# Kernel optimization log

Measured on AMD Instinct MI355X. Metric: run time of the kernel, lower is better.

## Reference

```python
import jax, jax.numpy as jnp
import numpy as np

CAPACITY_GAMMA = 0.5

def setup_inputs() -> dict:
    key = jax.random.key(0)
    k1, k2 = jax.random.split(key)
    B, S, H = 4, 4096, 2048
    hidden_states = jax.random.normal(k1, (B, S, H), dtype=jnp.float32)
    gate_w = jax.random.normal(k2, (1, H), dtype=jnp.float32) * (1.0 / np.sqrt(H))
    return {"hidden_states": hidden_states, "gate_w": gate_w}

def reference(hidden_states, gate_w):
    # scores: [B, S] = Linear(H -> 1, no bias) then squeeze
    scores = jnp.einsum("bsh,h->bs", hidden_states, gate_w[0])
    B, S = scores.shape
    k = int(CAPACITY_GAMMA * S)
    if k >= S:
        mask = jnp.ones_like(scores)
    else:
        _, top_idx = jax.lax.top_k(scores, k)          # [B, k]
        batch_idx = jnp.arange(B)[:, None]              # [B, 1]
        mask = jnp.zeros_like(scores).at[batch_idx, top_idx].set(1.0)
    return (mask, scores)
```

## Files before the change

### kernel.cpp

```cpp
#include <hip/hip_runtime.h>

#define BB 4
#define SS 4096
#define HH 2048
#define KK 2048

typedef float f4 __attribute__((ext_vector_type(4)));


__device__ __forceinline__ void load_row(const f4* __restrict__ base, int lane,
                                         f4 (&buf)[8]) {
#pragma unroll
    for (int i = 0; i < 8; ++i)
        buf[i] = __builtin_nontemporal_load(&base[i * 64 + lane]);
}

__device__ __forceinline__ double dot_row(const f4 (&a)[8], const f4 (&g)[8]) {
    double ax = 0.0, ay = 0.0, az = 0.0, aw = 0.0;
#pragma unroll
    for (int i = 0; i < 8; ++i) {
        ax = fma((double)a[i].x, (double)g[i].x, ax);
        ay = fma((double)a[i].y, (double)g[i].y, ay);
        az = fma((double)a[i].z, (double)g[i].z, az);
        aw = fma((double)a[i].w, (double)g[i].w, aw);
    }
    return (ax + ay) + (az + aw);
}

__device__ __forceinline__ void reduce_store(double acc, int lane, float* __restrict__ dst) {
#pragma unroll
    for (int off = 32; off >= 1; off >>= 1)
        acc += __shfl_down(acc, off);
    if (lane == 0) *dst = (float)acc;
}

__global__ void __launch_bounds__(256)
scores_kernel(const float* __restrict__ hs,
              const float* __restrict__ gw,
              float* __restrict__ scores) {
    int wave = threadIdx.x >> 6;
    int lane = threadIdx.x & 63;
    int row0 = blockIdx.x * 16 + wave * 4;

    const f4* g4 = reinterpret_cast<const f4*>(gw);
    f4 g[8];
#pragma unroll
    for (int i = 0; i < 8; ++i) g[i] = g4[i * 64 + lane];

    const f4* r0 = reinterpret_cast<const f4*>(hs + (size_t)row0 * HH);
    f4 A[8], B[8];
    load_row(r0 + 0 * 512, lane, A);
    load_row(r0 + 1 * 512, lane, B);
    double d0 = dot_row(A, g);
    load_row(r0 + 2 * 512, lane, A);
    double d1 = dot_row(B, g);
    load_row(r0 + 3 * 512, lane, B);
    double d2 = dot_row(A, g);
    double d3 = dot_row(B, g);

    reduce_store(d0, lane, scores + row0 + 0);
    reduce_store(d1, lane, scores + row0 + 1);
    reduce_store(d2, lane, scores + row0 + 2);
    reduce_store(d3, lane, scores + row0 + 3);
}


__device__ __forceinline__ unsigned to_ord(float f) {
    unsigned u = __float_as_uint(f);
    return (u & 0x80000000u) ? ~u : (u | 0x80000000u);
}

__device__ __forceinline__ int dpp_wave_sum(int v) {
    v += __builtin_amdgcn_update_dpp(0, v, 0x111, 0xF, 0xF, true);
    v += __builtin_amdgcn_update_dpp(0, v, 0x112, 0xF, 0xF, true);
    v += __builtin_amdgcn_update_dpp(0, v, 0x114, 0xF, 0xF, true);
    v += __builtin_amdgcn_update_dpp(0, v, 0x118, 0xF, 0xF, true);
    v += __builtin_amdgcn_update_dpp(0, v, 0x142, 0xF, 0xF, true);
    v += __builtin_amdgcn_update_dpp(0, v, 0x143, 0xF, 0xF, true);
    return __builtin_amdgcn_readlane(v, 63);
}

__global__ void __launch_bounds__(256)
topk_mask_kernel(const float* __restrict__ scores, float* __restrict__ mask) {
    int b = blockIdx.x, t = threadIdx.x;
    int w = t >> 6, lane = t & 63;
    const f4* sc4 = reinterpret_cast<const f4*>(scores + b * SS);

    f4 v[4];
#pragma unroll
    for (int i = 0; i < 4; ++i) v[i] = sc4[t * 4 + i];

    unsigned ord[16];
#pragma unroll
    for (int i = 0; i < 4; ++i) {
        ord[4 * i + 0] = to_ord(v[i].x);
        ord[4 * i + 1] = to_ord(v[i].y);
        ord[4 * i + 2] = to_ord(v[i].z);
        ord[4 * i + 3] = to_ord(v[i].w);
    }

    __shared__ int wsum[2][4];
    __shared__ int tts[256];

    unsigned cur = 0u, thresh = 0u;
    bool exact = false;
    int par = 0;
    for (int bit = 31; bit >= 0; --bit) {
        unsigned cand = cur | (1u << bit);
        int c = 0;
#pragma unroll
        for (int i = 0; i < 16; ++i) c += (ord[i] >= cand) ? 1 : 0;
        int ws = dpp_wave_sum(c);
        if (lane == 0) wsum[par][w] = ws;
        __syncthreads();
        int total = wsum[par][0] + wsum[par][1] + wsum[par][2] + wsum[par][3];
        par ^= 1;
        if (total >= KK) cur = cand;
        if (total == KK) { exact = true; thresh = cand; break; }
    }

    f4* m4 = reinterpret_cast<f4*>(mask + b * SS);

    if (exact) {
#pragma unroll
        for (int i = 0; i < 4; ++i) {
            f4 m;
            m.x = (ord[4 * i + 0] >= thresh) ? 1.0f : 0.0f;
            m.y = (ord[4 * i + 1] >= thresh) ? 1.0f : 0.0f;
            m.z = (ord[4 * i + 2] >= thresh) ? 1.0f : 0.0f;
            m.w = (ord[4 * i + 3] >= thresh) ? 1.0f : 0.0f;
            m4[t * 4 + i] = m;
        }
        return;
    }

    int cgl = 0, ttl = 0;
#pragma unroll
    for (int i = 0; i < 16; ++i) {
        cgl += (ord[i] > cur) ? 1 : 0;
        ttl += (ord[i] == cur) ? 1 : 0;
    }
    int cgw = dpp_wave_sum(cgl);
    if (lane == 0) wsum[0][w] = cgw;
    tts[t] = ttl;
    __syncthreads();
    int cg = wsum[0][0] + wsum[0][1] + wsum[0][2] + wsum[0][3];
    int r = KK - cg;
    if (t == 0) {
        int acc = 0;
        for (int i = 0; i < 256; ++i) { int x = tts[i]; tts[i] = acc; acc += x; }
    }
    __syncthreads();
    int pfx = tts[t];
#pragma unroll
    for (int i = 0; i < 4; ++i) {
        float mm[4];
#pragma unroll
        for (int j = 0; j < 4; ++j) {
            unsigned o = ord[4 * i + j];
            bool gt  = o > cur;
            bool tie = o == cur;
            mm[j] = (gt || (tie && pfx < r)) ? 1.0f : 0.0f;
            if (tie) ++pfx;
        }
        f4 m; m.x = mm[0]; m.y = mm[1]; m.z = mm[2]; m.w = mm[3];
        m4[t * 4 + i] = m;
    }
}

extern "C" void kernel_launch(void* const* d_in, const int* in_sizes, int n_in,
                              void* d_out, int out_size, void* d_ws, size_t ws_size,
                              hipStream_t stream) {
    const float* hs = (const float*)d_in[0];
    const float* gw = (const float*)d_in[1];
    float* out    = (float*)d_out;
    float* mask   = out;
    float* scores = out + BB * SS;

    scores_kernel<<<BB * SS / 16, 256, 0, stream>>>(hs, gw, scores);
    topk_mask_kernel<<<BB, 256, 0, stream>>>(scores, mask);
}
```

Before: 31.32 us.

## Split each wave into four 16-lane row groups and stage gate in LDS

The scores kernel now has each 16-lane group of a wave own one row, so a wave processes four rows concurrently rather than four rows in sequence. The gate vector is staged in shared memory and read per chunk instead of being held in registers. The cross-lane reduction shrinks to four xor shuffles within the group. Launch bounds request 4 blocks per SM to raise occupancy, at the cost of LDS reads and narrower 256-byte contiguous segments per group load.

```diff
diff --git a/kernel.cpp b/kernel.cpp
--- a/kernel.cpp
+++ b/kernel.cpp
@@ -8,60 +8,56 @@
 typedef float f4 __attribute__((ext_vector_type(4)));
 
 
-__device__ __forceinline__ void load_row(const f4* __restrict__ base, int lane,
-                                         f4 (&buf)[8]) {
-#pragma unroll
-    for (int i = 0; i < 8; ++i)
-        buf[i] = __builtin_nontemporal_load(&base[i * 64 + lane]);
-}
-
-__device__ __forceinline__ double dot_row(const f4 (&a)[8], const f4 (&g)[8]) {
-    double ax = 0.0, ay = 0.0, az = 0.0, aw = 0.0;
-#pragma unroll
-    for (int i = 0; i < 8; ++i) {
-        ax = fma((double)a[i].x, (double)g[i].x, ax);
-        ay = fma((double)a[i].y, (double)g[i].y, ay);
-        az = fma((double)a[i].z, (double)g[i].z, az);
-        aw = fma((double)a[i].w, (double)g[i].w, aw);
-    }
-    return (ax + ay) + (az + aw);
-}
-
-__device__ __forceinline__ void reduce_store(double acc, int lane, float* __restrict__ dst) {
-#pragma unroll
-    for (int off = 32; off >= 1; off >>= 1)
-        acc += __shfl_down(acc, off);
-    if (lane == 0) *dst = (float)acc;
-}
-
-__global__ void __launch_bounds__(256)
+__global__ void __launch_bounds__(256, 4)
 scores_kernel(const float* __restrict__ hs,
               const float* __restrict__ gw,
               float* __restrict__ scores) {
-    int wave = threadIdx.x >> 6;
-    int lane = threadIdx.x & 63;
-    int row0 = blockIdx.x * 16 + wave * 4;
+    __shared__ f4 gls[512];
+    int t = threadIdx.x;
+    const f4* g4 = reinterpret_cast<const f4*>(gw);
+    gls[t]       = g4[t];
+    gls[t + 256] = g4[t + 256];
+    __syncthreads();
 
-    const f4* g4 = reinterpret_cast<const f4*>(gw);
-    f4 g[8];
+    int wave = t >> 6, lane = t & 63;
+    int g = lane >> 4, p = lane & 15;
+    int row = blockIdx.x * 16 + wave * 4 + g;
+    const f4* r4 = reinterpret_cast<const f4*>(hs + (size_t)row * HH);
+
+    f4 A[8], B[8];
 #pragma unroll
-    for (int i = 0; i < 8; ++i) g[i] = g4[i * 64 + lane];
+    for (int i = 0; i < 8; ++i)
+        A[i] = __builtin_nontemporal_load(&r4[i * 16 + p]);
 
-    const f4* r0 = reinterpret_cast<const f4*>(hs + (size_t)row0 * HH);
-    f4 A[8], B[8];
-    load_row(r0 + 0 * 512, lane, A);
-    load_row(r0 + 1 * 512, lane, B);
-    double d0 = dot_row(A, g);
-    load_row(r0 + 2 * 512, lane, A);
-    double d1 = dot_row(B, g);
-    load_row(r0 + 3 * 512, lane, B);
-    double d2 = dot_row(A, g);
-    double d3 = dot_row(B, g);
+    double acc0 = 0.0, acc1 = 0.0;
+#pragma unroll
+    for (int c = 0; c < 4; ++c) {
+        if (c < 3) {
+#pragma unroll
+            for (int i = 0; i < 8; ++i)
+                B[i] = __builtin_nontemporal_load(&r4[(c + 1) * 128 + i * 16 + p]);
+        }
+#pragma unroll
+        for (int i = 0; i < 8; ++i) {
+            f4 gg = gls[c * 128 + i * 16 + p];
+            f4 aa = A[i];
+            acc0 = fma((double)aa.x, (double)gg.x, acc0);
+            acc1 = fma((double)aa.y, (double)gg.y, acc1);
+            acc0 = fma((double)aa.z, (double)gg.z, acc0);
+            acc1 = fma((double)aa.w, (double)gg.w, acc1);
+        }
+        if (c < 3) {
+#pragma unroll
+            for (int i = 0; i < 8; ++i) A[i] = B[i];
+        }
+    }
 
-    reduce_store(d0, lane, scores + row0 + 0);
-    reduce_store(d1, lane, scores + row0 + 1);
-    reduce_store(d2, lane, scores + row0 + 2);
-    reduce_store(d3, lane, scores + row0 + 3);
+    double s = acc0 + acc1;
+    s += __shfl_xor(s, 8);
+    s += __shfl_xor(s, 4);
+    s += __shfl_xor(s, 2);
+    s += __shfl_xor(s, 1);
+    if (p == 0) scores[row] = (float)s;
 }
 
 
```

New measurement: 32.48 us. 1.04x slower.

## Fuse score and top-k kernels using per-batch last-block atomic counter

Applied to the files above, without the earlier changes.

Merges the scores GEMV and the top-k mask kernel into one launch. Each block writes its scores and then increments a per-batch atomic counter, and the last block to finish for a batch runs the radix-select top-k for that batch. This removes a kernel launch and the gap between the two kernels, so the top-k for early batches can overlap with score computation for later ones. It adds a memset of the counters and relies on fences and atomics for cross-block visibility of the scores.

```diff
diff --git a/kernel.cpp b/kernel.cpp
--- a/kernel.cpp
+++ b/kernel.cpp
@@ -34,36 +34,6 @@
     if (lane == 0) *dst = (float)acc;
 }
 
-__global__ void __launch_bounds__(256)
-scores_kernel(const float* __restrict__ hs,
-              const float* __restrict__ gw,
-              float* __restrict__ scores) {
-    int wave = threadIdx.x >> 6;
-    int lane = threadIdx.x & 63;
-    int row0 = blockIdx.x * 16 + wave * 4;
-
-    const f4* g4 = reinterpret_cast<const f4*>(gw);
-    f4 g[8];
-#pragma unroll
-    for (int i = 0; i < 8; ++i) g[i] = g4[i * 64 + lane];
-
-    const f4* r0 = reinterpret_cast<const f4*>(hs + (size_t)row0 * HH);
-    f4 A[8], B[8];
-    load_row(r0 + 0 * 512, lane, A);
-    load_row(r0 + 1 * 512, lane, B);
-    double d0 = dot_row(A, g);
-    load_row(r0 + 2 * 512, lane, A);
-    double d1 = dot_row(B, g);
-    load_row(r0 + 3 * 512, lane, B);
-    double d2 = dot_row(A, g);
-    double d3 = dot_row(B, g);
-
-    reduce_store(d0, lane, scores + row0 + 0);
-    reduce_store(d1, lane, scores + row0 + 1);
-    reduce_store(d2, lane, scores + row0 + 2);
-    reduce_store(d3, lane, scores + row0 + 3);
-}
-
 
 __device__ __forceinline__ unsigned to_ord(float f) {
     unsigned u = __float_as_uint(f);
@@ -80,10 +50,51 @@
     return __builtin_amdgcn_readlane(v, 63);
 }
 
-__global__ void __launch_bounds__(256)
-topk_mask_kernel(const float* __restrict__ scores, float* __restrict__ mask) {
-    int b = blockIdx.x, t = threadIdx.x;
-    int w = t >> 6, lane = t & 63;
+__global__ void __launch_bounds__(256, 4)
+fused_kernel(const float* __restrict__ hs, const float* __restrict__ gw,
+             float* __restrict__ scores, float* __restrict__ mask,
+             int* __restrict__ cnt) {
+    int t = threadIdx.x;
+    int wave = t >> 6, lane = t & 63;
+    int row0 = blockIdx.x * 16 + wave * 4;
+
+    {
+        const f4* g4 = reinterpret_cast<const f4*>(gw);
+        f4 g[8];
+#pragma unroll
+        for (int i = 0; i < 8; ++i) g[i] = g4[i * 64 + lane];
+
+        const f4* r0 = reinterpret_cast<const f4*>(hs + (size_t)row0 * HH);
+        f4 A[8], B[8];
+        load_row(r0 + 0 * 512, lane, A);
+        load_row(r0 + 1 * 512, lane, B);
+        double d0 = dot_row(A, g);
+        load_row(r0 + 2 * 512, lane, A);
+        double d1 = dot_row(B, g);
+        load_row(r0 + 3 * 512, lane, B);
+        double d2 = dot_row(A, g);
+        double d3 = dot_row(B, g);
+
+        reduce_store(d0, lane, scores + row0 + 0);
+        reduce_store(d1, lane, scores + row0 + 1);
+        reduce_store(d2, lane, scores + row0 + 2);
+        reduce_store(d3, lane, scores + row0 + 3);
+    }
+
+    int b = blockIdx.x >> 8;
+    __shared__ int lastf;
+    __syncthreads();
+    if (t == 0) {
+        __threadfence();
+        int old = __hip_atomic_fetch_add(&cnt[b], 1, __ATOMIC_ACQ_REL,
+                                         __HIP_MEMORY_SCOPE_AGENT);
+        lastf = (old == BB * SS / 16 / BB - 1);
+    }
+    __syncthreads();
+    if (!lastf) return;
+    __threadfence();
+
+    int w = wave;
     const f4* sc4 = reinterpret_cast<const f4*>(scores + b * SS);
 
     f4 v[4];
@@ -176,7 +187,8 @@
     float* out    = (float*)d_out;
     float* mask   = out;
     float* scores = out + BB * SS;
+    int* cnt = (int*)d_ws;
 
-    scores_kernel<<<BB * SS / 16, 256, 0, stream>>>(hs, gw, scores);
-    topk_mask_kernel<<<BB, 256, 0, stream>>>(scores, mask);
+    hipMemsetAsync(cnt, 0, BB * sizeof(int), stream);
+    fused_kernel<<<BB * SS / 16, 256, 0, stream>>>(hs, gw, scores, mask, cnt);
 }
```

After: 107.5 us. +243.2%, slower.
